# Optimization experiments

Measured on AMD Instinct MI355X. Metric: run time of the kernel, lower is better.

## Reference

```python
import jax, jax.numpy as jnp
import numpy as np


def _l2norm(x, axis=-1, eps=1e-12):
    # matches F.normalize(p=2): x / max(||x||, eps)
    n = jnp.sqrt(jnp.sum(x * x, axis=axis, keepdims=True))
    return x / jnp.maximum(n, eps)


def setup_inputs() -> dict:
    key = jax.random.key(0)
    k1, k2 = jax.random.split(key)
    B, D, C = 262144, 256, 1000
    features = jax.random.normal(k1, (B, D), dtype=jnp.float32)
    labels = jax.random.randint(k2, (B,), 0, C, dtype=jnp.int64)
    return {"features": features, "labels": labels, "num_classes": C}


def reference(features, labels, num_classes):
    labels = labels.astype(jnp.int32)
    f = _l2norm(features, axis=1)  # (B, D)
    # per-class scatter-mean (classes with zero samples contribute no loss terms)
    sums = jax.ops.segment_sum(f, labels, num_segments=num_classes)      # (C, D)
    counts = jax.ops.segment_sum(jnp.ones((f.shape[0],), f.dtype), labels,
                                 num_segments=num_classes)               # (C,)
    protos = sums / jnp.maximum(counts, 1.0)[:, None]
    protos = _l2norm(protos, axis=1)                                     # (C, D)
    # cosine distance of each sample to its own class prototype
    p = protos[labels]                                                   # (B, D)
    dist = 1.0 - jnp.sum(f * p, axis=1)                                  # (B,)
    B = f.shape[0]
    return jnp.sum(dist) / jnp.maximum(B, 1)
```

## Files before the change

kernel.cpp:

```cpp
#include <hip/hip_runtime.h>


#define DIM 256
#define NB 64
#define SSB 2048

typedef float fx4 __attribute__((ext_vector_type(4)));

__global__ __launch_bounds__(256) void k_hist(const int* __restrict__ labels,
                                              int* __restrict__ hist,
                                              float* __restrict__ sums,
                                              int B, int C, int CD) {
  extern __shared__ int s_h[];
  const int tid = threadIdx.x;
  for (int i = blockIdx.x * 256 + tid; i < CD; i += NB * 256) sums[i] = 0.f;
  for (int c = tid; c < C; c += 256) s_h[c] = 0;
  __syncthreads();
  const int chunk = (B + NB - 1) / NB;
  const int r0 = blockIdx.x * chunk;
  const int r1 = min(B, r0 + chunk);
  for (int i = r0 + tid; i < r1; i += 256) atomicAdd(&s_h[labels[i]], 1);
  __syncthreads();
  int* dst = hist + (size_t)blockIdx.x * C;
  for (int c = tid; c < C; c += 256) dst[c] = s_h[c];
}

__global__ __launch_bounds__(1024) void k_scan(int* __restrict__ hist,
                                               float* __restrict__ out,
                                               unsigned* __restrict__ done,
                                               int C) {
  __shared__ int s[2][1024];
  const int tid = threadIdx.x;
  if (tid == 0) { out[0] = 0.f; *done = 0u; }
  int h[NB];
  int total = 0;
  if (tid < C) {
#pragma unroll
    for (int b = 0; b < NB; ++b) h[b] = hist[(size_t)b * C + tid];
#pragma unroll
    for (int b = 0; b < NB; ++b) {
      const int t = h[b];
      h[b] = total;
      total += t;
    }
  }
  int cur = 0;
  s[0][tid] = total;
  __syncthreads();
  for (int d = 1; d < 1024; d <<= 1) {
    const int v = s[cur][tid] + (tid >= d ? s[cur][tid - d] : 0);
    s[1 - cur][tid] = v;
    __syncthreads();
    cur ^= 1;
  }
  const int exoff = s[cur][tid] - total;
  if (tid < C) {
#pragma unroll
    for (int b = 0; b < NB; ++b) hist[(size_t)b * C + tid] = h[b] + exoff;
  }
}

__global__ __launch_bounds__(256) void k_permute(const int* __restrict__ labels,
                                                 const int* __restrict__ bases,
                                                 int2* __restrict__ pr,
                                                 int B, int C) {
  extern __shared__ int s_cur[];
  const int tid = threadIdx.x;
  const int* bp = bases + (size_t)blockIdx.x * C;
  for (int c = tid; c < C; c += 256) s_cur[c] = bp[c];
  __syncthreads();
  const int chunk = (B + NB - 1) / NB;
  const int r0 = blockIdx.x * chunk;
  const int r1 = min(B, r0 + chunk);
  for (int i = r0 + tid; i < r1; i += 256) {
    const int l = labels[i];
    const int pos = atomicAdd(&s_cur[l], 1);
    pr[pos] = make_int2(i, l);
  }
}

__device__ __forceinline__ void flush_acc(float* __restrict__ sums, int c,
                                          const fx4& a, int lane) {
  float* dst = sums + (size_t)c * DIM + lane * 4;
  atomicAdd(dst + 0, a.x);
  atomicAdd(dst + 1, a.y);
  atomicAdd(dst + 2, a.z);
  atomicAdd(dst + 3, a.w);
}

__global__ __launch_bounds__(256) void k_segsum(const float* __restrict__ x,
                                                const int2* __restrict__ pr,
                                                float* __restrict__ sums,
                                                int B) {
  const int lane = threadIdx.x & 63;
  const int wid = __builtin_amdgcn_readfirstlane(
      (blockIdx.x << 2) | (threadIdx.x >> 6));
  const int nw = SSB * 4;
  const int per = (B + nw - 1) / nw;
  const int r0 = wid * per;
  const int r1 = min(B, r0 + per);
  if (r0 >= r1) return;

  fx4 acc = {0.f, 0.f, 0.f, 0.f};
  int prev = -1;
  int rb = r0;

  for (; rb + 8 <= r1; rb += 8) {
    int2 e[8];
#pragma unroll
    for (int k = 0; k < 8; ++k) e[k] = pr[rb + k];
    fx4 v[8];
#pragma unroll
    for (int k = 0; k < 8; ++k)
      v[k] = __builtin_nontemporal_load(
          (const fx4*)(x + (size_t)e[k].x * DIM) + lane);
    float ss[8];
#pragma unroll
    for (int k = 0; k < 8; ++k)
      ss[k] = v[k].x * v[k].x + v[k].y * v[k].y + v[k].z * v[k].z +
              v[k].w * v[k].w;
#pragma unroll
    for (int off = 32; off; off >>= 1) {
#pragma unroll
      for (int k = 0; k < 8; ++k) ss[k] += __shfl_xor(ss[k], off);
    }
#pragma unroll
    for (int k = 0; k < 8; ++k) {
      const float inv = 1.f / fmaxf(sqrtf(ss[k]), 1e-12f);
      const int lab = e[k].y;
      if (lab != prev) {
        if (prev >= 0) flush_acc(sums, prev, acc, lane);
        acc = (fx4){0.f, 0.f, 0.f, 0.f};
        prev = lab;
      }
      acc.x += v[k].x * inv; acc.y += v[k].y * inv;
      acc.z += v[k].z * inv; acc.w += v[k].w * inv;
    }
  }
  for (; rb < r1; ++rb) {
    const int2 e = pr[rb];
    const fx4 v = ((const fx4*)(x + (size_t)e.x * DIM))[lane];
    float ss = v.x * v.x + v.y * v.y + v.z * v.z + v.w * v.w;
#pragma unroll
    for (int off = 32; off; off >>= 1) ss += __shfl_xor(ss, off);
    const float inv = 1.f / fmaxf(sqrtf(ss), 1e-12f);
    if (e.y != prev) {
      if (prev >= 0) flush_acc(sums, prev, acc, lane);
      acc = (fx4){0.f, 0.f, 0.f, 0.f};
      prev = e.y;
    }
    acc.x += v.x * inv; acc.y += v.y * inv;
    acc.z += v.z * inv; acc.w += v.w * inv;
  }
  if (prev >= 0) flush_acc(sums, prev, acc, lane);
}

__global__ __launch_bounds__(256) void k_norm(const float* __restrict__ sums,
                                              float* __restrict__ out,
                                              unsigned* __restrict__ done,
                                              int C, int B) {
  const int wave = threadIdx.x >> 6;
  const int lane = threadIdx.x & 63;
  const int c = blockIdx.x * 4 + wave;
  float term = 0.f;
  if (c < C) {
    const fx4 v = ((const fx4*)(sums + (size_t)c * DIM))[lane];
    float ss = v.x * v.x + v.y * v.y + v.z * v.z + v.w * v.w;
#pragma unroll
    for (int off = 32; off; off >>= 1) ss += __shfl_xor(ss, off);
    term = sqrtf(ss);
  }
  __shared__ float sp[4];
  if (lane == 0) sp[wave] = term;
  __syncthreads();
  if (threadIdx.x == 0) {
    atomicAdd(out, sp[0] + sp[1] + sp[2] + sp[3]);
    __threadfence();
    const unsigned d = atomicAdd(done, 1u);
    if (d == gridDim.x - 1) {
      const float t = atomicAdd(out, 0.f);
      out[0] = 1.f - t / (float)B;
    }
  }
}

extern "C" void kernel_launch(void* const* d_in, const int* in_sizes, int n_in,
                              void* d_out, int out_size, void* d_ws, size_t ws_size,
                              hipStream_t stream) {
  const float* x      = (const float*)d_in[0];
  const int*   labels = (const int*)d_in[1];
  const int B = in_sizes[1];
  const int C = 1000;

  char* ws = (char*)d_ws;
  int*      hist = (int*)ws;
  unsigned* done = (unsigned*)(ws + (size_t)NB * C * sizeof(int));
  size_t off = (((size_t)NB * C + 1) * sizeof(int) + 15) & ~(size_t)15;
  int2*  pr   = (int2*)(ws + off);
  off += (size_t)B * sizeof(int2);
  float* sums = (float*)(ws + off);

  const size_t lds_c = (size_t)C * sizeof(int);
  k_hist<<<NB, 256, lds_c, stream>>>(labels, hist, sums, B, C, C * DIM);
  k_scan<<<1, 1024, 0, stream>>>(hist, (float*)d_out, done, C);
  k_permute<<<NB, 256, lds_c, stream>>>(labels, hist, pr, B, C);
  k_segsum<<<SSB, 256, 0, stream>>>(x, pr, sums, B);
  const int nblk = (C + 3) / 4;
  k_norm<<<nblk, 256, 0, stream>>>(sums, (float*)d_out, done, C, B);
}
```

Measured before the change: 385.4 us.

## Store only row indices, derive class bounds from offsets, and prefetch next batch

```diff
diff --git a/kernel.cpp b/kernel.cpp
--- a/kernel.cpp
+++ b/kernel.cpp
@@ -26,6 +26,7 @@
 }
 
 __global__ __launch_bounds__(1024) void k_scan(int* __restrict__ hist,
+                                               int* __restrict__ offsets,
                                                float* __restrict__ out,
                                                unsigned* __restrict__ done,
                                                int C) {
@@ -54,6 +55,7 @@
     cur ^= 1;
   }
   const int exoff = s[cur][tid] - total;
+  if (tid <= C) offsets[tid] = exoff;
   if (tid < C) {
 #pragma unroll
     for (int b = 0; b < NB; ++b) hist[(size_t)b * C + tid] = h[b] + exoff;
@@ -62,7 +64,7 @@
 
 __global__ __launch_bounds__(256) void k_permute(const int* __restrict__ labels,
                                                  const int* __restrict__ bases,
-                                                 int2* __restrict__ pr,
+                                                 int* __restrict__ rows,
                                                  int B, int C) {
   extern __shared__ int s_cur[];
   const int tid = threadIdx.x;
@@ -75,7 +77,7 @@
   for (int i = r0 + tid; i < r1; i += 256) {
     const int l = labels[i];
     const int pos = atomicAdd(&s_cur[l], 1);
-    pr[pos] = make_int2(i, l);
+    rows[pos] = i;
   }
 }
 
@@ -89,9 +91,10 @@
 }
 
 __global__ __launch_bounds__(256) void k_segsum(const float* __restrict__ x,
-                                                const int2* __restrict__ pr,
+                                                const int* __restrict__ rows,
+                                                const int* __restrict__ offsets,
                                                 float* __restrict__ sums,
-                                                int B) {
+                                                int B, int C) {
   const int lane = threadIdx.x & 63;
   const int wid = __builtin_amdgcn_readfirstlane(
       (blockIdx.x << 2) | (threadIdx.x >> 6));
@@ -101,58 +104,77 @@
   const int r1 = min(B, r0 + per);
   if (r0 >= r1) return;
 
+  int lo = 0, hi = C;
+  while (hi - lo > 1) {
+    const int mid = (lo + hi) >> 1;
+    if (offsets[mid] <= r0) lo = mid; else hi = mid;
+  }
+  int c = lo;
+  int nextOff = offsets[c + 1];
+
   fx4 acc = {0.f, 0.f, 0.f, 0.f};
-  int prev = -1;
   int rb = r0;
 
-  for (; rb + 8 <= r1; rb += 8) {
-    int2 e[8];
-#pragma unroll
-    for (int k = 0; k < 8; ++k) e[k] = pr[rb + k];
+  if (rb + 8 <= r1) {
     fx4 v[8];
 #pragma unroll
     for (int k = 0; k < 8; ++k)
       v[k] = __builtin_nontemporal_load(
-          (const fx4*)(x + (size_t)e[k].x * DIM) + lane);
-    float ss[8];
-#pragma unroll
-    for (int k = 0; k < 8; ++k)
-      ss[k] = v[k].x * v[k].x + v[k].y * v[k].y + v[k].z * v[k].z +
-              v[k].w * v[k].w;
-#pragma unroll
-    for (int off = 32; off; off >>= 1) {
-#pragma unroll
-      for (int k = 0; k < 8; ++k) ss[k] += __shfl_xor(ss[k], off);
-    }
-#pragma unroll
-    for (int k = 0; k < 8; ++k) {
-      const float inv = 1.f / fmaxf(sqrtf(ss[k]), 1e-12f);
-      const int lab = e[k].y;
-      if (lab != prev) {
-        if (prev >= 0) flush_acc(sums, prev, acc, lane);
-        acc = (fx4){0.f, 0.f, 0.f, 0.f};
-        prev = lab;
-      }
-      acc.x += v[k].x * inv; acc.y += v[k].y * inv;
-      acc.z += v[k].z * inv; acc.w += v[k].w * inv;
+          (const fx4*)(x + (size_t)rows[rb + k] * DIM) + lane);
+    for (; rb + 8 <= r1; rb += 8) {
+      const bool more = (rb + 16 <= r1);
+      fx4 w[8];
+      if (more) {
+#pragma unroll
+        for (int k = 0; k < 8; ++k)
+          w[k] = __builtin_nontemporal_load(
+              (const fx4*)(x + (size_t)rows[rb + 8 + k] * DIM) + lane);
+      }
+      float ss[8];
+#pragma unroll
+      for (int k = 0; k < 8; ++k)
+        ss[k] = v[k].x * v[k].x + v[k].y * v[k].y + v[k].z * v[k].z +
+                v[k].w * v[k].w;
+#pragma unroll
+      for (int off = 32; off; off >>= 1) {
+#pragma unroll
+        for (int k = 0; k < 8; ++k) ss[k] += __shfl_xor(ss[k], off);
+      }
+#pragma unroll
+      for (int k = 0; k < 8; ++k) {
+        const float inv = 1.f / fmaxf(sqrtf(ss[k]), 1e-12f);
+        const int p = rb + k;
+        if (p >= nextOff) {
+          flush_acc(sums, c, acc, lane);
+          acc = (fx4){0.f, 0.f, 0.f, 0.f};
+          do { ++c; } while (offsets[c + 1] <= p);
+          nextOff = offsets[c + 1];
+        }
+        acc.x += v[k].x * inv; acc.y += v[k].y * inv;
+        acc.z += v[k].z * inv; acc.w += v[k].w * inv;
+      }
+      if (more) {
+#pragma unroll
+        for (int k = 0; k < 8; ++k) v[k] = w[k];
+      }
     }
   }
   for (; rb < r1; ++rb) {
-    const int2 e = pr[rb];
-    const fx4 v = ((const fx4*)(x + (size_t)e.x * DIM))[lane];
+    const fx4 v = ((const fx4*)(x + (size_t)rows[rb] * DIM))[lane];
     float ss = v.x * v.x + v.y * v.y + v.z * v.z + v.w * v.w;
 #pragma unroll
     for (int off = 32; off; off >>= 1) ss += __shfl_xor(ss, off);
     const float inv = 1.f / fmaxf(sqrtf(ss), 1e-12f);
-    if (e.y != prev) {
-      if (prev >= 0) flush_acc(sums, prev, acc, lane);
+    if (rb >= nextOff) {
+      flush_acc(sums, c, acc, lane);
       acc = (fx4){0.f, 0.f, 0.f, 0.f};
-      prev = e.y;
+      do { ++c; } while (offsets[c + 1] <= rb);
+      nextOff = offsets[c + 1];
     }
     acc.x += v.x * inv; acc.y += v.y * inv;
     acc.z += v.z * inv; acc.w += v.w * inv;
   }
-  if (prev >= 0) flush_acc(sums, prev, acc, lane);
+  flush_acc(sums, c, acc, lane);
 }
 
 __global__ __launch_bounds__(256) void k_norm(const float* __restrict__ sums,
@@ -193,18 +215,21 @@
   const int C = 1000;
 
   char* ws = (char*)d_ws;
-  int*      hist = (int*)ws;
-  unsigned* done = (unsigned*)(ws + (size_t)NB * C * sizeof(int));
-  size_t off = (((size_t)NB * C + 1) * sizeof(int) + 15) & ~(size_t)15;
-  int2*  pr   = (int2*)(ws + off);
-  off += (size_t)B * sizeof(int2);
+  int* hist = (int*)ws;
+  size_t off = (size_t)NB * C * sizeof(int);
+  int* offsets = (int*)(ws + off);
+  off += (size_t)(C + 1) * sizeof(int);
+  unsigned* done = (unsigned*)(ws + off);
+  off = (off + sizeof(int) + 15) & ~(size_t)15;
+  int* rows = (int*)(ws + off);
+  off += (size_t)B * sizeof(int);
   float* sums = (float*)(ws + off);
 
   const size_t lds_c = (size_t)C * sizeof(int);
   k_hist<<<NB, 256, lds_c, stream>>>(labels, hist, sums, B, C, C * DIM);
-  k_scan<<<1, 1024, 0, stream>>>(hist, (float*)d_out, done, C);
-  k_permute<<<NB, 256, lds_c, stream>>>(labels, hist, pr, B, C);
-  k_segsum<<<SSB, 256, 0, stream>>>(x, pr, sums, B);
+  k_scan<<<1, 1024, 0, stream>>>(hist, offsets, (float*)d_out, done, C);
+  k_permute<<<NB, 256, lds_c, stream>>>(labels, hist, rows, B, C);
+  k_segsum<<<SSB, 256, 0, stream>>>(x, rows, offsets, sums, B, C);
   const int nblk = (C + 3) / 4;
   k_norm<<<nblk, 256, 0, stream>>>(sums, (float*)d_out, done, C, B);
 }
```

New measurement: 378.5 us. About the same (-1.8%).
